# Kernel optimization log

Hardware: AMD Instinct MI355X
Metric: run time of the kernel (lower is better)

## Reference

```python
import jax, jax.numpy as jnp
import numpy as np

D_MODEL = 1024
H = 16
D_K = D_MODEL // H  # 64
B, S = 2, 2048


def setup_inputs() -> dict:
    key = jax.random.key(0)
    ks = jax.random.split(key, 8)
    scale = 1.0 / np.sqrt(D_MODEL)
    return {
        "q": jax.random.normal(ks[0], (B, S, D_MODEL), dtype=jnp.float32),
        "k": jax.random.normal(ks[1], (B, S, D_MODEL), dtype=jnp.float32),
        "v": jax.random.normal(ks[2], (B, S, D_MODEL), dtype=jnp.float32),
        "W_q": jax.random.normal(ks[3], (H, D_MODEL, D_K), dtype=jnp.float32) * scale,
        "W_k": jax.random.normal(ks[4], (H, D_MODEL, D_K), dtype=jnp.float32) * scale,
        "W_v": jax.random.normal(ks[5], (H, D_MODEL, D_K), dtype=jnp.float32) * scale,
        "W_o": jax.random.normal(ks[6], (D_MODEL, H * D_K), dtype=jnp.float32) * scale,
        "b_o": jnp.zeros((D_MODEL,), dtype=jnp.float32),
    }


def reference(q, k, v, W_q, W_k, W_v, W_o, b_o):
    b, s, _ = q.shape
    h, _, d_k = W_q.shape
    inv_sqrt_dk = jnp.asarray(1.0 / np.sqrt(d_k), q.dtype)
    # per-head projections: [b, h, s, d_k]
    qh = jnp.einsum("bsd,hdk->bhsk", q, W_q)
    kh = jnp.einsum("bsd,hdk->bhsk", k, W_k)
    vh = jnp.einsum("bsd,hdk->bhsk", v, W_v)
    # scaled dot product attention
    scores = jnp.einsum("bhqk,bhsk->bhqs", qh, kh) * inv_sqrt_dk  # [b,h,S,S]
    attn = jax.nn.softmax(scores, axis=-1)
    ctx = jnp.einsum("bhqs,bhsk->bhqk", attn, vh)  # [b,h,S,d_k]
    # chunk over heads + concat along feature dim -> [b, S, h*d_k], head-major
    ctx = ctx.transpose(0, 2, 1, 3).reshape(b, s, h * d_k)
    # final linear
    return ctx @ W_o.T + b_o
```

## Files before the change

### kernel.cpp

```cpp
#include <hip/hip_runtime.h>
#include <cstdint>
#include <cstddef>


typedef unsigned short bf16_t;
typedef __attribute__((ext_vector_type(8))) short short8;
typedef __attribute__((ext_vector_type(4))) float f32x4;

#define GLB_AS(p) ((const __attribute__((address_space(1))) void*)(p))
#define LDS_AS(p) ((__attribute__((address_space(3))) void*)(p))

__device__ __forceinline__ uint32_t fbits(float f) {
  union { float f; uint32_t u; } v; v.f = f; return v.u;
}
__device__ __forceinline__ bf16_t f2bf(float f) {
  uint32_t u = fbits(f);
  return (bf16_t)((u + 0x7FFFu + ((u >> 16) & 1u)) >> 16);
}
__device__ __forceinline__ uint32_t packbf2(float lo, float hi) {
  uint32_t a = fbits(hi) + 0x8000u;
  uint32_t b = fbits(lo) + 0x8000u;
  return __builtin_amdgcn_perm(a, b, 0x07060302u);
}

__global__ void prep_kernel(const float* __restrict__ q, const float* __restrict__ k,
                            const float* __restrict__ v, const float* __restrict__ Wo,
                            const float* __restrict__ Wq, const float* __restrict__ Wk,
                            const float* __restrict__ Wv,
                            bf16_t* __restrict__ qo, bf16_t* __restrict__ ko,
                            bf16_t* __restrict__ vo, bf16_t* __restrict__ Woo,
                            bf16_t* __restrict__ Wtq, bf16_t* __restrict__ Wtk,
                            bf16_t* __restrict__ Wtv) {
  int blk = blockIdx.x;
  int tid = threadIdx.x;
  if (blk < 13312) {
    const float* src; bf16_t* dst; int i;
    if (blk < 4096)       { src = q;  dst = qo;  i = blk * 256 + tid; }
    else if (blk < 8192)  { src = k;  dst = ko;  i = (blk - 4096) * 256 + tid; }
    else if (blk < 12288) { src = v;  dst = vo;  i = (blk - 8192) * 256 + tid; }
    else                  { src = Wo; dst = Woo; i = (blk - 12288) * 256 + tid; }
    f32x4 val = ((const f32x4*)src)[i];
    ushort4 o;
    o.x = f2bf(val.x); o.y = f2bf(val.y); o.z = f2bf(val.z); o.w = f2bf(val.w);
    ((ushort4*)dst)[i] = o;
  } else {
    int blk2 = blk - 13312;
    int z = blk2 >> 9, t = blk2 & 511;
    const float* W = z == 0 ? Wq : z == 1 ? Wk : Wv;
    bf16_t* Wt = z == 0 ? Wtq : z == 1 ? Wtk : Wtv;
    int h = t >> 5, d0 = (t & 31) * 32;
    __shared__ float tile[32][65];
    const float* src = W + ((size_t)h << 16) + (size_t)d0 * 64;
    int d = tid >> 3;
#pragma unroll
    for (int j = 0; j < 2; j++) {
      int dk = (tid & 7) * 8 + j * 4;
      *(f32x4*)&tile[d][dk] = *(const f32x4*)(src + d * 64 + dk);
    }
    __syncthreads();
    int dk2 = tid >> 2, c = tid & 3;
    union { ushort s[8]; int4 v; } o;
#pragma unroll
    for (int j = 0; j < 8; j++) o.s[j] = f2bf(tile[c * 8 + j][dk2]);
    *(int4*)(Wt + (size_t)(h * 64 + dk2) * 1024 + d0 + c * 8) = o.v;
  }
}

__global__ __launch_bounds__(256) void gemm_proj_kernel(
    const bf16_t* __restrict__ A0, const bf16_t* __restrict__ A1, const bf16_t* __restrict__ A2,
    const bf16_t* __restrict__ B0, const bf16_t* __restrict__ B1, const bf16_t* __restrict__ B2,
    bf16_t* __restrict__ O0, bf16_t* __restrict__ O1, bf16_t* __restrict__ O2,
    float s0)
{
  const int z = blockIdx.z;
  const bf16_t* A  = z == 0 ? A0 : z == 1 ? A1 : A2;
  const bf16_t* Bt = z == 0 ? B0 : z == 1 ? B1 : B2;
  bf16_t* Cout     = z == 0 ? O0 : z == 1 ? O1 : O2;
  const float scale = z == 0 ? s0 : 1.0f;
  const int K = 1024;

  __shared__ alignas(16) bf16_t smem[128 * 72];
  bf16_t* Asmem = smem;
  bf16_t* Bsmem = smem + 128 * 32;

  const int tid = threadIdx.x;
  const int lane = tid & 63, wave = tid >> 6;
  const int wm = wave >> 1, wn = wave & 1;
  const int quad = lane >> 4, l15 = lane & 15;
  const int m0 = blockIdx.y * 128, n0 = blockIdx.x * 128;

  f32x4 acc[4][4];
#pragma unroll
  for (int i = 0; i < 4; i++)
#pragma unroll
    for (int j = 0; j < 4; j++) acc[i][j] = (f32x4)0.0f;

  const int c0 = wave * 128 + lane;
  const int c1 = wave * 128 + 64 + lane;

  for (int k0 = 0; k0 < K; k0 += 32) {
    __builtin_amdgcn_global_load_lds(GLB_AS(A  + (size_t)(m0 + (c0 >> 2)) * K + k0 + (c0 & 3) * 8),
                                     LDS_AS(Asmem + c0 * 8), 16, 0, 0);
    __builtin_amdgcn_global_load_lds(GLB_AS(A  + (size_t)(m0 + (c1 >> 2)) * K + k0 + (c1 & 3) * 8),
                                     LDS_AS(Asmem + c1 * 8), 16, 0, 0);
    __builtin_amdgcn_global_load_lds(GLB_AS(Bt + (size_t)(n0 + (c0 >> 2)) * K + k0 + (c0 & 3) * 8),
                                     LDS_AS(Bsmem + c0 * 8), 16, 0, 0);
    __builtin_amdgcn_global_load_lds(GLB_AS(Bt + (size_t)(n0 + (c1 >> 2)) * K + k0 + (c1 & 3) * 8),
                                     LDS_AS(Bsmem + c1 * 8), 16, 0, 0);
    __syncthreads();

    short8 af[4], bfr[4];
#pragma unroll
    for (int mi = 0; mi < 4; mi++)
      af[mi] = *(const short8*)(Asmem + (wm * 64 + mi * 16 + l15) * 32 + quad * 8);
#pragma unroll
    for (int ni = 0; ni < 4; ni++)
      bfr[ni] = *(const short8*)(Bsmem + (wn * 64 + ni * 16 + l15) * 32 + quad * 8);
#pragma unroll
    for (int mi = 0; mi < 4; mi++)
#pragma unroll
      for (int ni = 0; ni < 4; ni++)
        acc[mi][ni] = __builtin_amdgcn_mfma_f32_16x16x32_bf16(af[mi], bfr[ni], acc[mi][ni], 0, 0, 0);
    __syncthreads();
  }

  const int s0r = m0 & 2047, bb = m0 >> 11;
  if (z < 2) {
#pragma unroll
    for (int p = 0; p < 2; p++) {
      if (wn == p) {
#pragma unroll
        for (int ni = 0; ni < 4; ni++)
#pragma unroll
          for (int mi = 0; mi < 4; mi++)
#pragma unroll
            for (int r = 0; r < 4; r++)
              smem[(wm * 64 + mi * 16 + quad * 4 + r) * 72 + ni * 16 + l15] =
                  f2bf(acc[mi][ni][r] * scale);
      }
      __syncthreads();
      int hp = (n0 >> 6) + p;
      bf16_t* dstbase = Cout + (((size_t)(bb * 16 + hp)) * 2048 + s0r) * 64;
#pragma unroll
      for (int rd = 0; rd < 4; rd++) {
        int idx = rd * 256 + tid;
        int m = idx >> 3, c8 = idx & 7;
        int4 val = *(const int4*)(smem + m * 72 + c8 * 8);
        *(int4*)(dstbase + (size_t)m * 64 + c8 * 8) = val;
      }
      __syncthreads();
    }
  } else {
#pragma unroll
    for (int p = 0; p < 2; p++) {
      if (wn == p) {
#pragma unroll
        for (int ni = 0; ni < 4; ni++)
#pragma unroll
          for (int mi = 0; mi < 4; mi++) {
            uint2 pk = make_uint2(packbf2(acc[mi][ni][0], acc[mi][ni][1]),
                                  packbf2(acc[mi][ni][2], acc[mi][ni][3]));
            *(uint2*)(smem + (ni * 16 + l15) * 136 + wm * 64 + mi * 16 + quad * 4) = pk;
          }
      }
      __syncthreads();
      int hp = (n0 >> 6) + p;
      bf16_t* dstbase = Cout + ((size_t)(bb * 16 + hp)) * 64 * 2048 + s0r;
#pragma unroll
      for (int rd = 0; rd < 4; rd++) {
        int idx = rd * 256 + tid;
        int c = idx >> 4, ck = idx & 15;
        int4 val = *(const int4*)(smem + c * 136 + ck * 8);
        *(int4*)(dstbase + (size_t)c * 2048 + ck * 8) = val;
      }
      __syncthreads();
    }
  }
}

__global__ __launch_bounds__(256) void gemm_out_kernel(
    const bf16_t* __restrict__ A, const bf16_t* __restrict__ Bt,
    float* __restrict__ C, const float* __restrict__ bias)
{
  const int K = 1024, N = 1024;
  __shared__ alignas(16) bf16_t Asmem[128 * 32];
  __shared__ alignas(16) bf16_t Bsmem[64 * 32];
  const int tid = threadIdx.x;
  const int lane = tid & 63, wave = tid >> 6;
  const int quad = lane >> 4, l15 = lane & 15;
  const int m0 = blockIdx.y * 128, n0 = blockIdx.x * 64;

  f32x4 acc[2][4];
#pragma unroll
  for (int i = 0; i < 2; i++)
#pragma unroll
    for (int j = 0; j < 4; j++) acc[i][j] = (f32x4)0.0f;

  const int c0 = wave * 128 + lane;
  const int c1 = wave * 128 + 64 + lane;
  const int cb = wave * 64 + lane;

  for (int k0 = 0; k0 < K; k0 += 32) {
    __builtin_amdgcn_global_load_lds(GLB_AS(A  + (size_t)(m0 + (c0 >> 2)) * K + k0 + (c0 & 3) * 8),
                                     LDS_AS(Asmem + c0 * 8), 16, 0, 0);
    __builtin_amdgcn_global_load_lds(GLB_AS(A  + (size_t)(m0 + (c1 >> 2)) * K + k0 + (c1 & 3) * 8),
                                     LDS_AS(Asmem + c1 * 8), 16, 0, 0);
    __builtin_amdgcn_global_load_lds(GLB_AS(Bt + (size_t)(n0 + (cb >> 2)) * K + k0 + (cb & 3) * 8),
                                     LDS_AS(Bsmem + cb * 8), 16, 0, 0);
    __syncthreads();

    short8 af[2], bfr[4];
#pragma unroll
    for (int mi = 0; mi < 2; mi++)
      af[mi] = *(const short8*)(Asmem + (wave * 32 + mi * 16 + l15) * 32 + quad * 8);
#pragma unroll
    for (int ni = 0; ni < 4; ni++)
      bfr[ni] = *(const short8*)(Bsmem + (ni * 16 + l15) * 32 + quad * 8);
#pragma unroll
    for (int mi = 0; mi < 2; mi++)
#pragma unroll
      for (int ni = 0; ni < 4; ni++)
        acc[mi][ni] = __builtin_amdgcn_mfma_f32_16x16x32_bf16(af[mi], bfr[ni], acc[mi][ni], 0, 0, 0);
    __syncthreads();
  }

#pragma unroll
  for (int ni = 0; ni < 4; ni++) {
    int col = n0 + ni * 16 + l15;
    float bv = bias[col];
#pragma unroll
    for (int mi = 0; mi < 2; mi++) {
      int row = m0 + wave * 32 + mi * 16 + quad * 4;
#pragma unroll
      for (int r = 0; r < 4; r++)
        C[(size_t)(row + r) * N + col] = acc[mi][ni][r] + bv;
    }
  }
}

__global__ __launch_bounds__(512) void flash_kernel(
    const bf16_t* __restrict__ qh, const bf16_t* __restrict__ kh,
    const bf16_t* __restrict__ vT, bf16_t* __restrict__ ctx)
{
  __shared__ alignas(16) bf16_t KtF[2][4096];
  __shared__ alignas(16) bf16_t VtF[2][4096];
  __shared__ alignas(16) bf16_t PtF[8 * 1024];
  const int tid = threadIdx.x, lane = tid & 63, wave = tid >> 6;
  const int quad = lane >> 4, l15 = lane & 15;
  const int q0 = blockIdx.x * 128;
  const int h = blockIdx.y, b = blockIdx.z;
  const size_t headoff = (size_t)(b * 16 + h) * 2048 * 64;
  const bf16_t* Q = qh + headoff;
  const bf16_t* K = kh + headoff;
  const bf16_t* V = vT + headoff;

  const int qrow = q0 + wave * 16 + l15;
  short8 qf[2];
#pragma unroll
  for (int ks = 0; ks < 2; ks++)
    qf[ks] = *(const short8*)(Q + (size_t)qrow * 64 + ks * 32 + quad * 8);

  f32x4 O[4];
#pragma unroll
  for (int mi = 0; mi < 4; mi++) O[mi] = (f32x4)0.0f;
  f32x4 lacc = (f32x4)0.0f;

  const bf16_t* Kp = K + (size_t)((wave >> 1) * 16 + l15) * 64 + (wave & 1) * 32 + quad * 8;
  const bf16_t* Vp = V + (size_t)((wave >> 1) * 16 + l15) * 2048 + (wave & 1) * 32 + quad * 8;
  const int soff = wave * 512 + lane * 8;

  const int pwbase = wave * 2048 + ((quad >> 1) * 16 + l15) * 16 + 8 * (quad & 1);

  int4 kreg = *(const int4*)Kp;
  int4 vreg = *(const int4*)Vp;
  *(int4*)(&KtF[0][soff]) = kreg;
  *(int4*)(&VtF[0][soff]) = vreg;
  __syncthreads();

  for (int it = 0; it < 32; ++it) {
    const int cur = it & 1, nxt = cur ^ 1;
    if (it < 31) {
      kreg = *(const int4*)(Kp + (size_t)(it + 1) * 4096);
      vreg = *(const int4*)(Vp + (it + 1) * 64);
    }

    f32x4 S[4];
#pragma unroll
    for (int mi = 0; mi < 4; mi++) S[mi] = (f32x4)0.0f;
#pragma unroll
    for (int ks = 0; ks < 2; ks++) {
#pragma unroll
      for (int mi = 0; mi < 4; mi++) {
        short8 kf = *(const short8*)(&KtF[cur][(mi * 2 + ks) * 512 + lane * 8]);
        S[mi] = __builtin_amdgcn_mfma_f32_16x16x32_bf16(kf, qf[ks], S[mi], 0, 0, 0);
      }
    }

#pragma unroll
    for (int mi = 0; mi < 4; mi++)
#pragma unroll
      for (int r = 0; r < 4; r++)
        S[mi][r] = __builtin_amdgcn_exp2f(S[mi][r]);
    lacc += (S[0] + S[1]) + (S[2] + S[3]);

#pragma unroll
    for (int mi = 0; mi < 4; mi++) {
      uint2 pk = make_uint2(packbf2(S[mi][0], S[mi][1]), packbf2(S[mi][2], S[mi][3]));
      *(uint2*)((char*)PtF + pwbase + (mi >> 1) * 1024 + (mi & 1) * 512) = pk;
    }

#pragma unroll
    for (int ks = 0; ks < 2; ks++) {
      short8 pfrag = *(const short8*)(&PtF[wave * 1024 + (ks * 64 + lane) * 8]);
#pragma unroll
      for (int mi = 0; mi < 4; mi++) {
        short8 vf = *(const short8*)(&VtF[cur][(mi * 2 + ks) * 512 + lane * 8]);
        O[mi] = __builtin_amdgcn_mfma_f32_16x16x32_bf16(vf, pfrag, O[mi], 0, 0, 0);
      }
    }

    if (it < 31) {
      *(int4*)(&KtF[nxt][soff]) = kreg;
      *(int4*)(&VtF[nxt][soff]) = vreg;
    }
    __syncthreads();
  }

  float l = (lacc[0] + lacc[1]) + (lacc[2] + lacc[3]);
  l += __shfl_xor(l, 16, 64);
  l += __shfl_xor(l, 32, 64);
  float inv = 1.0f / l;
  bf16_t* crow = ctx + ((size_t)(b * 2048 + qrow)) * 1024 + h * 64;
#pragma unroll
  for (int mi = 0; mi < 4; mi++) {
    uint2 pk = make_uint2(packbf2(O[mi][0] * inv, O[mi][1] * inv),
                          packbf2(O[mi][2] * inv, O[mi][3] * inv));
    *(uint2*)(crow + mi * 16 + quad * 4) = pk;
  }
}

extern "C" void kernel_launch(void* const* d_in, const int* in_sizes, int n_in,
                              void* d_out, int out_size, void* d_ws, size_t ws_size,
                              hipStream_t stream)
{
  const float* q  = (const float*)d_in[0];
  const float* k  = (const float*)d_in[1];
  const float* v  = (const float*)d_in[2];
  const float* Wq = (const float*)d_in[3];
  const float* Wk = (const float*)d_in[4];
  const float* Wv = (const float*)d_in[5];
  const float* Wo = (const float*)d_in[6];
  const float* bo = (const float*)d_in[7];
  float* out = (float*)d_out;

  const size_t NX = (size_t)4096 * 1024;
  const size_t NW = (size_t)1024 * 1024;

  char* p = (char*)d_ws;
  bf16_t* qbf = (bf16_t*)p; p += NX * 2;
  bf16_t* kbf = (bf16_t*)p; p += NX * 2;
  bf16_t* vbf = (bf16_t*)p; p += NX * 2;
  bf16_t* Wtq = (bf16_t*)p; p += NW * 2;
  bf16_t* Wtk = (bf16_t*)p; p += NW * 2;
  bf16_t* Wtv = (bf16_t*)p; p += NW * 2;
  bf16_t* Wob = (bf16_t*)p; p += NW * 2;
  bf16_t* qhb = (bf16_t*)p; p += NX * 2;
  bf16_t* khb = (bf16_t*)p; p += NX * 2;
  bf16_t* vTb = (bf16_t*)p; p += NX * 2;
  bf16_t* ctxb = (bf16_t*)p; p += NX * 2;

  prep_kernel<<<14848, 256, 0, stream>>>(q, k, v, Wo, Wq, Wk, Wv,
                                         qbf, kbf, vbf, Wob, Wtq, Wtk, Wtv);

  const float qscale = 0.125f * 1.44269504088896340736f;
  gemm_proj_kernel<<<dim3(8, 32, 3), 256, 0, stream>>>(qbf, kbf, vbf, Wtq, Wtk, Wtv,
                                                       qhb, khb, vTb, qscale);

  flash_kernel<<<dim3(16, 16, 2), 512, 0, stream>>>(qhb, khb, vTb, ctxb);

  gemm_out_kernel<<<dim3(16, 32), 256, 0, stream>>>(ctxb, Wob, out, bo);

  (void)in_sizes; (void)n_in; (void)out_size; (void)ws_size;
}
```

Baseline: 231.0 us.

## Double-buffer LDS via register prefetch in projection and output GEMMs

The direct global-to-LDS loads in both GEMM kernels are replaced with register-staged prefetch. The next K-slice is loaded into registers while the current slice runs through MFMA, then written into an alternate LDS buffer, so each iteration needs only one barrier instead of two. The projection epilogue also writes both head halves into separate LDS slots at once and stores them in one pass, removing a loop and its barriers. In exchange it uses more LDS and registers, which may reduce occupancy.

```diff
diff --git a/kernel.cpp b/kernel.cpp
--- a/kernel.cpp
+++ b/kernel.cpp
@@ -6,9 +6,6 @@
 typedef unsigned short bf16_t;
 typedef __attribute__((ext_vector_type(8))) short short8;
 typedef __attribute__((ext_vector_type(4))) float f32x4;
-
-#define GLB_AS(p) ((const __attribute__((address_space(1))) void*)(p))
-#define LDS_AS(p) ((__attribute__((address_space(3))) void*)(p))
 
 __device__ __forceinline__ uint32_t fbits(float f) {
   union { float f; uint32_t u; } v; v.f = f; return v.u;
@@ -79,9 +76,7 @@
   const float scale = z == 0 ? s0 : 1.0f;
   const int K = 1024;
 
-  __shared__ alignas(16) bf16_t smem[128 * 72];
-  bf16_t* Asmem = smem;
-  bf16_t* Bsmem = smem + 128 * 32;
+  __shared__ alignas(16) bf16_t smem[18432];
 
   const int tid = threadIdx.x;
   const int lane = tid & 63, wave = tid >> 6;
@@ -96,84 +91,92 @@
     for (int j = 0; j < 4; j++) acc[i][j] = (f32x4)0.0f;
 
   const int c0 = wave * 128 + lane;
-  const int c1 = wave * 128 + 64 + lane;
-
-  for (int k0 = 0; k0 < K; k0 += 32) {
-    __builtin_amdgcn_global_load_lds(GLB_AS(A  + (size_t)(m0 + (c0 >> 2)) * K + k0 + (c0 & 3) * 8),
-                                     LDS_AS(Asmem + c0 * 8), 16, 0, 0);
-    __builtin_amdgcn_global_load_lds(GLB_AS(A  + (size_t)(m0 + (c1 >> 2)) * K + k0 + (c1 & 3) * 8),
-                                     LDS_AS(Asmem + c1 * 8), 16, 0, 0);
-    __builtin_amdgcn_global_load_lds(GLB_AS(Bt + (size_t)(n0 + (c0 >> 2)) * K + k0 + (c0 & 3) * 8),
-                                     LDS_AS(Bsmem + c0 * 8), 16, 0, 0);
-    __builtin_amdgcn_global_load_lds(GLB_AS(Bt + (size_t)(n0 + (c1 >> 2)) * K + k0 + (c1 & 3) * 8),
-                                     LDS_AS(Bsmem + c1 * 8), 16, 0, 0);
-    __syncthreads();
+  const int c1 = c0 + 64;
+  const bf16_t* pa0 = A  + (size_t)(m0 + (c0 >> 2)) * K + (c0 & 3) * 8;
+  const bf16_t* pa1 = A  + (size_t)(m0 + (c1 >> 2)) * K + (c1 & 3) * 8;
+  const bf16_t* pb0 = Bt + (size_t)(n0 + (c0 >> 2)) * K + (c0 & 3) * 8;
+  const bf16_t* pb1 = Bt + (size_t)(n0 + (c1 >> 2)) * K + (c1 & 3) * 8;
+  const int s0a = c0 * 8, s1a = c1 * 8;
+
+  int4 ra0 = *(const int4*)pa0;
+  int4 ra1 = *(const int4*)pa1;
+  int4 rb0 = *(const int4*)pb0;
+  int4 rb1 = *(const int4*)pb1;
+  *(int4*)(smem + s0a) = ra0;
+  *(int4*)(smem + s1a) = ra1;
+  *(int4*)(smem + 4096 + s0a) = rb0;
+  *(int4*)(smem + 4096 + s1a) = rb1;
+  __syncthreads();
+
+  for (int it = 0; it < 32; ++it) {
+    const int co = (it & 1) * 8192;
+    if (it < 31) {
+      const int ko = (it + 1) * 32;
+      ra0 = *(const int4*)(pa0 + ko);
+      ra1 = *(const int4*)(pa1 + ko);
+      rb0 = *(const int4*)(pb0 + ko);
+      rb1 = *(const int4*)(pb1 + ko);
+    }
 
     short8 af[4], bfr[4];
 #pragma unroll
     for (int mi = 0; mi < 4; mi++)
-      af[mi] = *(const short8*)(Asmem + (wm * 64 + mi * 16 + l15) * 32 + quad * 8);
+      af[mi] = *(const short8*)(smem + co + (wm * 64 + mi * 16 + l15) * 32 + quad * 8);
 #pragma unroll
     for (int ni = 0; ni < 4; ni++)
-      bfr[ni] = *(const short8*)(Bsmem + (wn * 64 + ni * 16 + l15) * 32 + quad * 8);
+      bfr[ni] = *(const short8*)(smem + co + 4096 + (wn * 64 + ni * 16 + l15) * 32 + quad * 8);
 #pragma unroll
     for (int mi = 0; mi < 4; mi++)
 #pragma unroll
       for (int ni = 0; ni < 4; ni++)
         acc[mi][ni] = __builtin_amdgcn_mfma_f32_16x16x32_bf16(af[mi], bfr[ni], acc[mi][ni], 0, 0, 0);
-    __syncthreads();
-  }
-
-  const int s0r = m0 & 2047, bb = m0 >> 11;
+
+    if (it < 31) {
+      const int no = ((it + 1) & 1) * 8192;
+      *(int4*)(smem + no + s0a) = ra0;
+      *(int4*)(smem + no + s1a) = ra1;
+      *(int4*)(smem + no + 4096 + s0a) = rb0;
+      *(int4*)(smem + no + 4096 + s1a) = rb1;
+    }
+    __syncthreads();
+  }
+
+  const int s0r = m0 & 2047, bb = m0 >> 11, hp = n0 >> 6;
   if (z < 2) {
-#pragma unroll
-    for (int p = 0; p < 2; p++) {
-      if (wn == p) {
-#pragma unroll
-        for (int ni = 0; ni < 4; ni++)
-#pragma unroll
-          for (int mi = 0; mi < 4; mi++)
-#pragma unroll
-            for (int r = 0; r < 4; r++)
-              smem[(wm * 64 + mi * 16 + quad * 4 + r) * 72 + ni * 16 + l15] =
-                  f2bf(acc[mi][ni][r] * scale);
+    bf16_t* slot = smem + wn * 9216;
+#pragma unroll
+    for (int ni = 0; ni < 4; ni++)
+#pragma unroll
+      for (int mi = 0; mi < 4; mi++)
+#pragma unroll
+        for (int r = 0; r < 4; r++)
+          slot[(wm * 64 + mi * 16 + quad * 4 + r) * 72 + ni * 16 + l15] =
+              f2bf(acc[mi][ni][r] * scale);
+    __syncthreads();
+#pragma unroll
+    for (int rd = 0; rd < 8; ++rd) {
+      int idx = rd * 256 + tid;
+      int si = idx >> 10, mm = (idx >> 3) & 127, c8 = idx & 7;
+      int4 val = *(const int4*)(smem + si * 9216 + mm * 72 + c8 * 8);
+      *(int4*)(Cout + ((size_t)((bb * 16 + hp + si) * 2048 + s0r + mm)) * 64 + c8 * 8) = val;
+    }
+  } else {
+    bf16_t* slot = smem + wn * 8704;
+#pragma unroll
+    for (int ni = 0; ni < 4; ni++)
+#pragma unroll
+      for (int mi = 0; mi < 4; mi++) {
+        uint2 pk = make_uint2(packbf2(acc[mi][ni][0], acc[mi][ni][1]),
+                              packbf2(acc[mi][ni][2], acc[mi][ni][3]));
+        *(uint2*)(slot + (ni * 16 + l15) * 136 + wm * 64 + mi * 16 + quad * 4) = pk;
       }
-      __syncthreads();
-      int hp = (n0 >> 6) + p;
-      bf16_t* dstbase = Cout + (((size_t)(bb * 16 + hp)) * 2048 + s0r) * 64;
-#pragma unroll
-      for (int rd = 0; rd < 4; rd++) {
-        int idx = rd * 256 + tid;
-        int m = idx >> 3, c8 = idx & 7;
-        int4 val = *(const int4*)(smem + m * 72 + c8 * 8);
-        *(int4*)(dstbase + (size_t)m * 64 + c8 * 8) = val;
-      }
-      __syncthreads();
-    }
-  } else {
-#pragma unroll
-    for (int p = 0; p < 2; p++) {
-      if (wn == p) {
-#pragma unroll
-        for (int ni = 0; ni < 4; ni++)
-#pragma unroll
-          for (int mi = 0; mi < 4; mi++) {
-            uint2 pk = make_uint2(packbf2(acc[mi][ni][0], acc[mi][ni][1]),
-                                  packbf2(acc[mi][ni][2], acc[mi][ni][3]));
-            *(uint2*)(smem + (ni * 16 + l15) * 136 + wm * 64 + mi * 16 + quad * 4) = pk;
-          }
-      }
-      __syncthreads();
-      int hp = (n0 >> 6) + p;
-      bf16_t* dstbase = Cout + ((size_t)(bb * 16 + hp)) * 64 * 2048 + s0r;
-#pragma unroll
-      for (int rd = 0; rd < 4; rd++) {
-        int idx = rd * 256 + tid;
-        int c = idx >> 4, ck = idx & 15;
-        int4 val = *(const int4*)(smem + c * 136 + ck * 8);
-        *(int4*)(dstbase + (size_t)c * 2048 + ck * 8) = val;
-      }
-      __syncthreads();
+    __syncthreads();
+#pragma unroll
+    for (int rd = 0; rd < 8; ++rd) {
+      int idx = rd * 256 + tid;
+      int si = idx >> 10, c = (idx >> 4) & 63, ck = idx & 15;
+      int4 val = *(const int4*)(smem + si * 8704 + c * 136 + ck * 8);
+      *(int4*)(Cout + (size_t)(bb * 16 + hp + si) * 131072 + (size_t)c * 2048 + s0r + ck * 8) = val;
     }
   }
 }
@@ -183,8 +186,7 @@
     float* __restrict__ C, const float* __restrict__ bias)
 {
   const int K = 1024, N = 1024;
-  __shared__ alignas(16) bf16_t Asmem[128 * 32];
-  __shared__ alignas(16) bf16_t Bsmem[64 * 32];
+  __shared__ alignas(16) bf16_t smem[12288];
   const int tid = threadIdx.x;
   const int lane = tid & 63, wave = tid >> 6;
   const int quad = lane >> 4, l15 = lane & 15;
@@ -196,31 +198,49 @@
 #pragma unroll
     for (int j = 0; j < 4; j++) acc[i][j] = (f32x4)0.0f;
 
-  const int c0 = wave * 128 + lane;
-  const int c1 = wave * 128 + 64 + lane;
+  const int c0 = wave * 128 + lane, c1 = c0 + 64;
   const int cb = wave * 64 + lane;
-
-  for (int k0 = 0; k0 < K; k0 += 32) {
-    __builtin_amdgcn_global_load_lds(GLB_AS(A  + (size_t)(m0 + (c0 >> 2)) * K + k0 + (c0 & 3) * 8),
-                                     LDS_AS(Asmem + c0 * 8), 16, 0, 0);
-    __builtin_amdgcn_global_load_lds(GLB_AS(A  + (size_t)(m0 + (c1 >> 2)) * K + k0 + (c1 & 3) * 8),
-                                     LDS_AS(Asmem + c1 * 8), 16, 0, 0);
-    __builtin_amdgcn_global_load_lds(GLB_AS(Bt + (size_t)(n0 + (cb >> 2)) * K + k0 + (cb & 3) * 8),
-                                     LDS_AS(Bsmem + cb * 8), 16, 0, 0);
-    __syncthreads();
+  const bf16_t* pa0 = A  + (size_t)(m0 + (c0 >> 2)) * K + (c0 & 3) * 8;
+  const bf16_t* pa1 = A  + (size_t)(m0 + (c1 >> 2)) * K + (c1 & 3) * 8;
+  const bf16_t* pb  = Bt + (size_t)(n0 + (cb >> 2)) * K + (cb & 3) * 8;
+  const int s0a = c0 * 8, s1a = c1 * 8, sba = cb * 8;
+
+  int4 ra0 = *(const int4*)pa0;
+  int4 ra1 = *(const int4*)pa1;
+  int4 rb  = *(const int4*)pb;
+  *(int4*)(smem + s0a) = ra0;
+  *(int4*)(smem + s1a) = ra1;
+  *(int4*)(smem + 4096 + sba) = rb;
+  __syncthreads();
+
+  for (int it = 0; it < 32; ++it) {
+    const int co = (it & 1) * 6144;
+    if (it < 31) {
+      const int ko = (it + 1) * 32;
+      ra0 = *(const int4*)(pa0 + ko);
+      ra1 = *(const int4*)(pa1 + ko);
+      rb  = *(const int4*)(pb + ko);
+    }
 
     short8 af[2], bfr[4];
 #pragma unroll
     for (int mi = 0; mi < 2; mi++)
-      af[mi] = *(const short8*)(Asmem + (wave * 32 + mi * 16 + l15) * 32 + quad * 8);
+      af[mi] = *(const short8*)(smem + co + (wave * 32 + mi * 16 + l15) * 32 + quad * 8);
 #pragma unroll
     for (int ni = 0; ni < 4; ni++)
-      bfr[ni] = *(const short8*)(Bsmem + (ni * 16 + l15) * 32 + quad * 8);
+      bfr[ni] = *(const short8*)(smem + co + 4096 + (ni * 16 + l15) * 32 + quad * 8);
 #pragma unroll
     for (int mi = 0; mi < 2; mi++)
 #pragma unroll
       for (int ni = 0; ni < 4; ni++)
         acc[mi][ni] = __builtin_amdgcn_mfma_f32_16x16x32_bf16(af[mi], bfr[ni], acc[mi][ni], 0, 0, 0);
+
+    if (it < 31) {
+      const int no = ((it + 1) & 1) * 6144;
+      *(int4*)(smem + no + s0a) = ra0;
+      *(int4*)(smem + no + s1a) = ra1;
+      *(int4*)(smem + no + 4096 + sba) = rb;
+    }
     __syncthreads();
   }
 
```

Measured after the change: 217.6 us. 1.06x faster.
